# Performance work log

Hardware: AMD Instinct MI355X
Metric: run time of the kernel (lower is better)

Reference implementation:

```python
import jax, jax.numpy as jnp
import numpy as np

DIM = 16        # lagrangian.dim -> y has 2*DIM phase-space coords
HID = 128       # hidden width of the parametric Lagrangian
BATCH = 32768


def setup_inputs() -> dict:
    key = jax.random.key(0)
    k1, k2, k3, k4 = jax.random.split(key, 4)
    y = jax.random.normal(k1, (BATCH, 2 * DIM), dtype=jnp.float32)
    # small-scale init keeps J_{qdot,qdot} = I + (MLP Hessian block) well conditioned
    W1 = jax.random.normal(k2, (HID, 2 * DIM), dtype=jnp.float32) * (1.0 / np.sqrt(2 * DIM))
    b1 = jax.random.normal(k3, (HID,), dtype=jnp.float32) * 0.1
    w2 = jax.random.normal(k4, (HID,), dtype=jnp.float32) * 0.1
    return {"y": y, "W1": W1, "b1": b1, "w2": w2}


def _lagrangian(y_vec, W1, b1, w2):
    """Scalar Lagrangian L(q, qdot) for a single phase-space vector y_vec [2*DIM]."""
    qdot = y_vec[DIM:]
    kinetic = 0.5 * jnp.dot(qdot, qdot)
    return kinetic + jnp.dot(w2, jnp.tanh(W1 @ y_vec + b1))


def reference(y, W1, b1, w2):
    """Acceleration qdotdot = (dL/dq - qdot . J_{q,qdot}) . J_{qdot,qdot}^{-1}.

    Instead of the original O(dim^2) repeated tf.gradients calls, compute the
    full gradient and Hessian once per sample via fused forward-over-reverse
    autodiff, vmapped over the batch.
    """
    d = DIM
    L = lambda yv: _lagrangian(yv, W1, b1, w2)
    grad_fn = jax.grad(L)
    hess_fn = jax.jacfwd(grad_fn)  # forward-over-reverse Hessian, one sweep

    g = jax.vmap(grad_fn)(y)   # [B, 2d]   full dL/dy
    H = jax.vmap(hess_fn)(y)   # [B, 2d, 2d]  full Hessian d2L/(dy dy)

    qdot = y[:, d:]            # [B, d]
    dLdq = g[:, :d]            # [B, d]
    J_qqdot = H[:, :d, d:]     # [B, d, d]  d2L/(dq_i dqdot_j)
    J_qdqd_inv = jnp.linalg.inv(H[:, d:, d:])  # [B, d, d]

    rhs = dLdq - jnp.einsum('bi,bij->bj', qdot, J_qqdot)
    qdotdot = jnp.einsum('bi,bij->bj', rhs, J_qdqd_inv)
    return qdotdot
```

## Files before the change

kernel.cpp:

```cpp
#include <hip/hip_runtime.h>
#include <math.h>

#define DIMQ 16
#define HID  128
#define SPB  32
#define NTHREADS 512

typedef __attribute__((ext_vector_type(8))) _Float16 f16x8;
typedef __attribute__((ext_vector_type(4))) _Float16 f16x4;
typedef __attribute__((ext_vector_type(4))) float f32x4;
typedef __attribute__((ext_vector_type(2))) float v2f;

#define ASTR 280
#define USTR 280
#define SSTR 136

#define OFF_WFF  0
#define OFF_YFF  8192
#define OFF_ABT  10240
#define OFF_USP  19200
#define OFF_SST  37120
#define OFF_MSCR 0
#define LDS_BYTES 45824

__device__ __forceinline__ int mswz(int s, int off) {
    return s * 320 + (off ^ ((s & 7) << 2));
}
__device__ __forceinline__ f16x8 pack8(float4 a, float4 b) {
    f16x8 r;
    r[0]=(_Float16)a.x; r[1]=(_Float16)a.y; r[2]=(_Float16)a.z; r[3]=(_Float16)a.w;
    r[4]=(_Float16)b.x; r[5]=(_Float16)b.y; r[6]=(_Float16)b.z; r[7]=(_Float16)b.w;
    return r;
}

__global__ __launch_bounds__(NTHREADS, 4)
void lag_accel_kernel(const float* __restrict__ y,
                      const float* __restrict__ W1,
                      const float* __restrict__ b1,
                      const float* __restrict__ w2,
                      float* __restrict__ out)
{
    __shared__ __align__(16) char smem[LDS_BYTES];
    _Float16* Wff = (_Float16*)(smem + OFF_WFF);
    _Float16* Yff = (_Float16*)(smem + OFF_YFF);
    _Float16* ABT = (_Float16*)(smem + OFF_ABT);
    _Float16* usp = (_Float16*)(smem + OFF_USP);
    _Float16* sst = (_Float16*)(smem + OFF_SST);

    const int tid = threadIdx.x;
    const long long s0 = (long long)blockIdx.x * SPB;

    {
        const int ht_ = tid >> 6, grp_ = (tid >> 4) & 3, j_ = tid & 15;
        const float4* src = (const float4*)(W1 + (ht_ * 16 + j_) * 32 + (grp_ << 3));
        *(f16x8*)&Wff[tid * 8] = pack8(src[0], src[1]);
    }
    if (tid < 256) {
        const int st_ = tid >> 7, grp_ = (tid >> 5) & 3, j_ = (tid >> 1) & 15, hf = tid & 1;
        float4 v = *(const float4*)(y + (s0 + st_ * 16 + j_) * 32 + (grp_ << 3) + (hf << 2));
        f16x4 p; p[0]=(_Float16)v.x; p[1]=(_Float16)v.y; p[2]=(_Float16)v.z; p[3]=(_Float16)v.w;
        *(f16x4*)&Yff[(((st_ * 4 + grp_) * 16 + j_) << 3) + (hf << 2)] = p;
    }
    {
        const int k = tid & 31, h0 = (tid >> 5) << 3;
        float v[8];
#pragma unroll
        for (int i = 0; i < 8; ++i) v[i] = W1[(h0 + i) * 32 + k];
        f16x8 p;
#pragma unroll
        for (int i = 0; i < 8; ++i) p[i] = (_Float16)v[i];
        const int j_ = (k < 16) ? k : (k - 16);
        const int off = (k < 16) ? h0 : (128 + h0);
        *(f16x8*)&ABT[j_ * ASTR + off] = p;
    }

    const int wave = tid >> 6;
    const int lane = tid & 63;
    const int grp  = lane >> 4;
    const int j    = lane & 15;
    const int ht   = wave;

    float4 b1v = *(const float4*)&b1[ht * 16 + (grp << 2)];
    float4 w2v = *(const float4*)&w2[ht * 16 + (grp << 2)];

    __syncthreads();

    f16x8 aW  = *(const f16x8*)&Wff[((ht * 4 + grp) * 16 + j) * 8];
    f16x8 aAl = *(const f16x8*)&Wff[((ht * 4 + (grp & 1)) * 16 + j) * 8];
    f16x8 aA;
#pragma unroll
    for (int e = 0; e < 8; ++e) aA[e] = (grp >= 2) ? aAl[e] : (_Float16)0.0f;

    f32x4 zacc[2], aacc[2];
    {
        f32x4 ci; ci[0] = b1v.x; ci[1] = b1v.y; ci[2] = b1v.z; ci[3] = b1v.w;
        f32x4 zf = {0.0f, 0.0f, 0.0f, 0.0f};
        f16x8 yf0 = *(const f16x8*)&Yff[((0 * 4 + grp) * 16 + j) * 8];
        f16x8 yf1 = *(const f16x8*)&Yff[((1 * 4 + grp) * 16 + j) * 8];
        zacc[0] = __builtin_amdgcn_mfma_f32_16x16x32_f16(aW, yf0, ci, 0, 0, 0);
        zacc[1] = __builtin_amdgcn_mfma_f32_16x16x32_f16(aW, yf1, ci, 0, 0, 0);
        aacc[0] = __builtin_amdgcn_mfma_f32_16x16x32_f16(aA, yf0, zf, 0, 0, 0);
        aacc[1] = __builtin_amdgcn_mfma_f32_16x16x32_f16(aA, yf1, zf, 0, 0, 0);
    }

    const int h4 = ht * 16 + (grp << 2);
#define EWST(st)                                                         \
    {                                                                    \
        _Float16 su[4], sn[4], sv[4];                                    \
        _Pragma("unroll")                                                \
        for (int r = 0; r < 4; ++r) {                                    \
            float z  = zacc[st][r], aq = aacc[st][r];                    \
            float w2c = (r == 0) ? w2v.x : (r == 1) ? w2v.y               \
                       : (r == 2) ? w2v.z : w2v.w;                       \
            float e  = __expf(2.0f * z);                                 \
            float rr = 2.0f * __builtin_amdgcn_rcpf(e + 1.0f);           \
            float t  = 1.0f - rr;                                        \
            float u  = w2c * (rr * (2.0f - rr));                         \
            float s  = -2.0f * t * u;                                    \
            float sp = s * aq;                                           \
            su[r] = (_Float16)u; sn[r] = (_Float16)(-sp);                \
            sv[r] = (_Float16)s;                                         \
        }                                                                \
        const int smp2 = (st) * 16 + j;                                  \
        f16x4 pa = {su[0], su[1], su[2], su[3]};                         \
        f16x4 pb = {sn[0], sn[1], sn[2], sn[3]};                         \
        f16x4 pc = {sv[0], sv[1], sv[2], sv[3]};                         \
        *(f16x4*)&usp[smp2 * USTR + h4]       = pa;                      \
        *(f16x4*)&usp[smp2 * USTR + 128 + h4] = pb;                      \
        *(f16x4*)&sst[smp2 * SSTR + h4]       = pc;                      \
    }
    EWST(0)
    EWST(1)
#undef EWST

    __syncthreads();

    f32x4 racc = {0.0f, 0.0f, 0.0f, 0.0f};
    if (wave < 2) {
#pragma unroll
        for (int kc = 0; kc < 8; ++kc) {
            f16x8 af = *(const f16x8*)&ABT[j * ASTR + (kc << 5) + (grp << 3)];
            f16x8 bf = *(const f16x8*)&usp[(wave * 16 + j) * USTR + (kc << 5) + (grp << 3)];
            racc = __builtin_amdgcn_mfma_f32_16x16x32_f16(af, bf, racc, 0, 0, 0);
        }
    }

    f32x4 acc[4];
    {
        f32x4 ident;
#pragma unroll
        for (int r = 0; r < 4; ++r) ident[r] = ((grp << 2) + r == j) ? 1.0f : 0.0f;
#pragma unroll
        for (int gs = 0; gs < 4; ++gs) acc[gs] = ident;
    }
#pragma unroll
    for (int kc = 0; kc < 4; ++kc) {
        f16x8 bfrag = *(const f16x8*)&ABT[j * ASTR + 128 + (kc << 5) + (grp << 3)];
#pragma unroll
        for (int gs = 0; gs < 4; ++gs) {
            f16x8 sfrag = *(const f16x8*)&sst[(wave * 4 + gs) * SSTR + (kc << 5) + (grp << 3)];
            f16x8 afrag = sfrag * bfrag;
            acc[gs] = __builtin_amdgcn_mfma_f32_16x16x32_f16(afrag, bfrag, acc[gs], 0, 0, 0);
        }
    }

    __syncthreads();

    float* Mscr = (float*)(smem + OFF_MSCR);
#pragma unroll
    for (int gs = 0; gs < 4; ++gs) {
        float4 v;
        v.x = acc[gs][0]; v.y = acc[gs][1]; v.z = acc[gs][2]; v.w = acc[gs][3];
        *(float4*)&Mscr[mswz(wave * 4 + gs, j * 20 + (grp << 2))] = v;
    }

    __syncthreads();

    if (wave >= 2) return;
    const int sl = lane & 15;
    const int rb = lane >> 4;
    const int s  = wave * 16 + sl;

    v2f M2[4][8];
    float r4[4], d4[4];
#pragma unroll
    for (int r = 0; r < 4; ++r) {
        const int ro = (4 * rb + r) * 20;
        float4 v0 = *(const float4*)&Mscr[mswz(s, ro + 0)];
        float4 v1 = *(const float4*)&Mscr[mswz(s, ro + 4)];
        float4 v2 = *(const float4*)&Mscr[mswz(s, ro + 8)];
        float4 v3 = *(const float4*)&Mscr[mswz(s, ro + 12)];
        M2[r][0] = (v2f){v0.x, v0.y}; M2[r][1] = (v2f){v0.z, v0.w};
        M2[r][2] = (v2f){v1.x, v1.y}; M2[r][3] = (v2f){v1.z, v1.w};
        M2[r][4] = (v2f){v2.x, v2.y}; M2[r][5] = (v2f){v2.z, v2.w};
        M2[r][6] = (v2f){v3.x, v3.y}; M2[r][7] = (v2f){v3.z, v3.w};
        r4[r] = racc[r];
        d4[r] = 1.0f;
    }

#pragma unroll
    for (int k = 0; k < 16; ++k) {
        const int src = sl + ((k >> 2) << 4);
        float piv = __shfl(M2[k & 3][k >> 1][k & 1], src, 64);
        float rk  = __shfl(r4[k & 3], src, 64);
        float invp = __builtin_amdgcn_rcpf(piv);
        invp = invp * (2.0f - piv * invp);
        float f[4];
#pragma unroll
        for (int r = 0; r < 4; ++r) {
            float fr = M2[r][k >> 1][k & 1] * invp;
            const bool isk = ((rb << 2) + r) == k;
            f[r]  = isk ? 0.0f : fr;
            d4[r] = isk ? piv : d4[r];
            r4[r] = fmaf(-f[r], rk, r4[r]);
        }
        const int i2s = (k >> 1) + (k & 1);
#pragma unroll
        for (int i2 = i2s; i2 < 8; ++i2) {
            float p0 = (2 * i2 == k) ? piv : __shfl(M2[k & 3][i2][0], src, 64);
            float p1 = __shfl(M2[k & 3][i2][1], src, 64);
            v2f pv = {p0, p1};
#pragma unroll
            for (int r = 0; r < 4; ++r) {
                v2f fv = {-f[r], -f[r]};
                M2[r][i2] = __builtin_elementwise_fma(fv, pv, M2[r][i2]);
            }
        }
    }

    float4 xo;
    {
        float i0 = __builtin_amdgcn_rcpf(d4[0]); i0 = i0 * (2.0f - d4[0] * i0);
        float i1 = __builtin_amdgcn_rcpf(d4[1]); i1 = i1 * (2.0f - d4[1] * i1);
        float i2 = __builtin_amdgcn_rcpf(d4[2]); i2 = i2 * (2.0f - d4[2] * i2);
        float i3 = __builtin_amdgcn_rcpf(d4[3]); i3 = i3 * (2.0f - d4[3] * i3);
        xo.x = r4[0] * i0; xo.y = r4[1] * i1; xo.z = r4[2] * i2; xo.w = r4[3] * i3;
    }
    *(float4*)&out[(s0 + s) * DIMQ + (rb << 2)] = xo;
}

extern "C" void kernel_launch(void* const* d_in, const int* in_sizes, int n_in,
                              void* d_out, int out_size, void* d_ws, size_t ws_size,
                              hipStream_t stream) {
    const float* y  = (const float*)d_in[0];
    const float* W1 = (const float*)d_in[1];
    const float* b1 = (const float*)d_in[2];
    const float* w2 = (const float*)d_in[3];
    float* out = (float*)d_out;
    const int batch = in_sizes[0] / 32;
    const int blocks = (batch + SPB - 1) / SPB;
    lag_accel_kernel<<<blocks, NTHREADS, 0, stream>>>(y, W1, b1, w2, out);
}
```

Measured before the change: 19.21 us.

## Halve samples per block and have each wave cover two hidden tiles

Blocks now handle 16 samples with 256 threads instead of 32 samples with 512 threads. Each of the 4 waves computes two hidden-unit tiles against a single shared y fragment, and only wave 0 runs the RHS contraction and the 16x16 elimination. The goal is twice as many smaller blocks, which should spread better across CUs, use less LDS per block and idle fewer waves during the solve. The cost is that W1 is staged and converted once per block, so that redundant traffic and work doubles across the grid.

```diff
diff --git a/kernel.cpp b/kernel.cpp
--- a/kernel.cpp
+++ b/kernel.cpp
@@ -3,8 +3,8 @@
 
 #define DIMQ 16
 #define HID  128
-#define SPB  32
-#define NTHREADS 512
+#define SPB  16
+#define NTHREADS 256
 
 typedef __attribute__((ext_vector_type(8))) _Float16 f16x8;
 typedef __attribute__((ext_vector_type(4))) _Float16 f16x4;
@@ -17,11 +17,11 @@
 
 #define OFF_WFF  0
 #define OFF_YFF  8192
-#define OFF_ABT  10240
-#define OFF_USP  19200
-#define OFF_SST  37120
+#define OFF_ABT  9216
+#define OFF_USP  18176
+#define OFF_SST  27136
 #define OFF_MSCR 0
-#define LDS_BYTES 45824
+#define LDS_BYTES 31488
 
 __device__ __forceinline__ int mswz(int s, int off) {
     return s * 320 + (off ^ ((s & 7) << 2));
@@ -50,19 +50,23 @@
     const int tid = threadIdx.x;
     const long long s0 = (long long)blockIdx.x * SPB;
 
-    {
-        const int ht_ = tid >> 6, grp_ = (tid >> 4) & 3, j_ = tid & 15;
+#pragma unroll
+    for (int it = 0; it < 2; ++it) {
+        const int slot = tid + it * 256;
+        const int ht_ = slot >> 6, grp_ = (slot >> 4) & 3, j_ = slot & 15;
         const float4* src = (const float4*)(W1 + (ht_ * 16 + j_) * 32 + (grp_ << 3));
-        *(f16x8*)&Wff[tid * 8] = pack8(src[0], src[1]);
-    }
-    if (tid < 256) {
-        const int st_ = tid >> 7, grp_ = (tid >> 5) & 3, j_ = (tid >> 1) & 15, hf = tid & 1;
-        float4 v = *(const float4*)(y + (s0 + st_ * 16 + j_) * 32 + (grp_ << 3) + (hf << 2));
+        *(f16x8*)&Wff[slot * 8] = pack8(src[0], src[1]);
+    }
+    if (tid < 128) {
+        const int grp_ = (tid >> 5) & 3, j_ = (tid >> 1) & 15, hf = tid & 1;
+        float4 v = *(const float4*)(y + (s0 + j_) * 32 + (grp_ << 3) + (hf << 2));
         f16x4 p; p[0]=(_Float16)v.x; p[1]=(_Float16)v.y; p[2]=(_Float16)v.z; p[3]=(_Float16)v.w;
-        *(f16x4*)&Yff[(((st_ * 4 + grp_) * 16 + j_) << 3) + (hf << 2)] = p;
-    }
-    {
-        const int k = tid & 31, h0 = (tid >> 5) << 3;
+        *(f16x4*)&Yff[((grp_ * 16 + j_) << 3) + (hf << 2)] = p;
+    }
+#pragma unroll
+    for (int it = 0; it < 2; ++it) {
+        const int idx = tid + it * 256;
+        const int k = idx & 31, h0 = (idx >> 5) << 3;
         float v[8];
 #pragma unroll
         for (int i = 0; i < 8; ++i) v[i] = W1[(h0 + i) * 32 + k];
@@ -78,56 +82,53 @@
     const int lane = tid & 63;
     const int grp  = lane >> 4;
     const int j    = lane & 15;
-    const int ht   = wave;
-
-    float4 b1v = *(const float4*)&b1[ht * 16 + (grp << 2)];
-    float4 w2v = *(const float4*)&w2[ht * 16 + (grp << 2)];
-
-    __syncthreads();
-
-    f16x8 aW  = *(const f16x8*)&Wff[((ht * 4 + grp) * 16 + j) * 8];
-    f16x8 aAl = *(const f16x8*)&Wff[((ht * 4 + (grp & 1)) * 16 + j) * 8];
-    f16x8 aA;
-#pragma unroll
-    for (int e = 0; e < 8; ++e) aA[e] = (grp >= 2) ? aAl[e] : (_Float16)0.0f;
+
+    __syncthreads();
+
+    f16x8 yf = *(const f16x8*)&Yff[((grp * 16 + j) << 3)];
 
     f32x4 zacc[2], aacc[2];
-    {
+    float4 w2v[2];
+#pragma unroll
+    for (int t = 0; t < 2; ++t) {
+        const int ht = wave * 2 + t;
+        f16x8 aW  = *(const f16x8*)&Wff[((ht * 4 + grp) * 16 + j) * 8];
+        f16x8 aAl = *(const f16x8*)&Wff[((ht * 4 + (grp & 1)) * 16 + j) * 8];
+        f16x8 aA;
+#pragma unroll
+        for (int e = 0; e < 8; ++e) aA[e] = (grp >= 2) ? aAl[e] : (_Float16)0.0f;
+        float4 b1v = *(const float4*)&b1[ht * 16 + (grp << 2)];
+        w2v[t] = *(const float4*)&w2[ht * 16 + (grp << 2)];
         f32x4 ci; ci[0] = b1v.x; ci[1] = b1v.y; ci[2] = b1v.z; ci[3] = b1v.w;
         f32x4 zf = {0.0f, 0.0f, 0.0f, 0.0f};
-        f16x8 yf0 = *(const f16x8*)&Yff[((0 * 4 + grp) * 16 + j) * 8];
-        f16x8 yf1 = *(const f16x8*)&Yff[((1 * 4 + grp) * 16 + j) * 8];
-        zacc[0] = __builtin_amdgcn_mfma_f32_16x16x32_f16(aW, yf0, ci, 0, 0, 0);
-        zacc[1] = __builtin_amdgcn_mfma_f32_16x16x32_f16(aW, yf1, ci, 0, 0, 0);
-        aacc[0] = __builtin_amdgcn_mfma_f32_16x16x32_f16(aA, yf0, zf, 0, 0, 0);
-        aacc[1] = __builtin_amdgcn_mfma_f32_16x16x32_f16(aA, yf1, zf, 0, 0, 0);
-    }
-
-    const int h4 = ht * 16 + (grp << 2);
-#define EWST(st)                                                         \
+        zacc[t] = __builtin_amdgcn_mfma_f32_16x16x32_f16(aW, yf, ci, 0, 0, 0);
+        aacc[t] = __builtin_amdgcn_mfma_f32_16x16x32_f16(aA, yf, zf, 0, 0, 0);
+    }
+
+#define EWST(t)                                                          \
     {                                                                    \
+        const int h4 = (wave * 2 + (t)) * 16 + (grp << 2);               \
         _Float16 su[4], sn[4], sv[4];                                    \
         _Pragma("unroll")                                                \
         for (int r = 0; r < 4; ++r) {                                    \
-            float z  = zacc[st][r], aq = aacc[st][r];                    \
-            float w2c = (r == 0) ? w2v.x : (r == 1) ? w2v.y               \
-                       : (r == 2) ? w2v.z : w2v.w;                       \
+            float z  = zacc[t][r], aq = aacc[t][r];                      \
+            float w2c = (r == 0) ? w2v[t].x : (r == 1) ? w2v[t].y         \
+                       : (r == 2) ? w2v[t].z : w2v[t].w;                 \
             float e  = __expf(2.0f * z);                                 \
             float rr = 2.0f * __builtin_amdgcn_rcpf(e + 1.0f);           \
-            float t  = 1.0f - rr;                                        \
+            float t_ = 1.0f - rr;                                        \
             float u  = w2c * (rr * (2.0f - rr));                         \
-            float s  = -2.0f * t * u;                                    \
+            float s  = -2.0f * t_ * u;                                   \
             float sp = s * aq;                                           \
             su[r] = (_Float16)u; sn[r] = (_Float16)(-sp);                \
             sv[r] = (_Float16)s;                                         \
         }                                                                \
-        const int smp2 = (st) * 16 + j;                                  \
         f16x4 pa = {su[0], su[1], su[2], su[3]};                         \
         f16x4 pb = {sn[0], sn[1], sn[2], sn[3]};                         \
         f16x4 pc = {sv[0], sv[1], sv[2], sv[3]};                         \
-        *(f16x4*)&usp[smp2 * USTR + h4]       = pa;                      \
-        *(f16x4*)&usp[smp2 * USTR + 128 + h4] = pb;                      \
-        *(f16x4*)&sst[smp2 * SSTR + h4]       = pc;                      \
+        *(f16x4*)&usp[j * USTR + h4]       = pa;                         \
+        *(f16x4*)&usp[j * USTR + 128 + h4] = pb;                         \
+        *(f16x4*)&sst[j * SSTR + h4]       = pc;                         \
     }
     EWST(0)
     EWST(1)
@@ -136,11 +137,11 @@
     __syncthreads();
 
     f32x4 racc = {0.0f, 0.0f, 0.0f, 0.0f};
-    if (wave < 2) {
+    if (wave == 0) {
 #pragma unroll
         for (int kc = 0; kc < 8; ++kc) {
             f16x8 af = *(const f16x8*)&ABT[j * ASTR + (kc << 5) + (grp << 3)];
-            f16x8 bf = *(const f16x8*)&usp[(wave * 16 + j) * USTR + (kc << 5) + (grp << 3)];
+            f16x8 bf = *(const f16x8*)&usp[j * USTR + (kc << 5) + (grp << 3)];
             racc = __builtin_amdgcn_mfma_f32_16x16x32_f16(af, bf, racc, 0, 0, 0);
         }
     }
@@ -176,20 +177,19 @@
 
     __syncthreads();
 
-    if (wave >= 2) return;
+    if (wave != 0) return;
     const int sl = lane & 15;
     const int rb = lane >> 4;
-    const int s  = wave * 16 + sl;
 
     v2f M2[4][8];
     float r4[4], d4[4];
 #pragma unroll
     for (int r = 0; r < 4; ++r) {
         const int ro = (4 * rb + r) * 20;
-        float4 v0 = *(const float4*)&Mscr[mswz(s, ro + 0)];
-        float4 v1 = *(const float4*)&Mscr[mswz(s, ro + 4)];
-        float4 v2 = *(const float4*)&Mscr[mswz(s, ro + 8)];
-        float4 v3 = *(const float4*)&Mscr[mswz(s, ro + 12)];
+        float4 v0 = *(const float4*)&Mscr[mswz(sl, ro + 0)];
+        float4 v1 = *(const float4*)&Mscr[mswz(sl, ro + 4)];
+        float4 v2 = *(const float4*)&Mscr[mswz(sl, ro + 8)];
+        float4 v3 = *(const float4*)&Mscr[mswz(sl, ro + 12)];
         M2[r][0] = (v2f){v0.x, v0.y}; M2[r][1] = (v2f){v0.z, v0.w};
         M2[r][2] = (v2f){v1.x, v1.y}; M2[r][3] = (v2f){v1.z, v1.w};
         M2[r][4] = (v2f){v2.x, v2.y}; M2[r][5] = (v2f){v2.z, v2.w};
@@ -236,7 +236,7 @@
         float i3 = __builtin_amdgcn_rcpf(d4[3]); i3 = i3 * (2.0f - d4[3] * i3);
         xo.x = r4[0] * i0; xo.y = r4[1] * i1; xo.z = r4[2] * i2; xo.w = r4[3] * i3;
     }
-    *(float4*)&out[(s0 + s) * DIMQ + (rb << 2)] = xo;
+    *(float4*)&out[(s0 + sl) * DIMQ + (rb << 2)] = xo;
 }
 
 extern "C" void kernel_launch(void* const* d_in, const int* in_sizes, int n_in,
```

Result: slower. 20.78 us (+8.2%).
